# Performance work log

Measured on AMD Instinct MI355X. Metric: run time of the kernel, lower is better.

## Reference

```python
import jax, jax.numpy as jnp
from jax import lax
import numpy as np

NUM_LABELS = 48
BATCH, SEQ_LEN = 512, 1024


def setup_inputs() -> dict:
    key = jax.random.key(0)
    k1, k2, k3, k4, k5 = jax.random.split(key, 5)
    emissions = jax.random.normal(k1, (BATCH, SEQ_LEN, NUM_LABELS), dtype=jnp.float32)
    labels = jax.random.randint(k2, (BATCH, SEQ_LEN), 0, NUM_LABELS, dtype=jnp.int32)
    mask = jnp.ones((BATCH, SEQ_LEN), dtype=jnp.int32)
    transitions = jax.random.normal(k3, (NUM_LABELS, NUM_LABELS), dtype=jnp.float32)
    start_transitions = jax.random.normal(k4, (NUM_LABELS,), dtype=jnp.float32)
    end_transitions = jax.random.normal(k5, (NUM_LABELS,), dtype=jnp.float32)
    return {
        "emissions": emissions,
        "labels": labels,
        "mask": mask,
        "transitions": transitions,
        "start_transitions": start_transitions,
        "end_transitions": end_transitions,
    }


def _gold_score(emissions, labels, mask, transitions, start_transitions, end_transitions):
    maskf = mask.astype(emissions.dtype)
    # emissions gathered at gold labels: (B, T)
    emit = jnp.take_along_axis(emissions, labels[..., None], axis=2)[..., 0]
    # NOTE: original indexes transitions[labels_t, labels_{t-1}] (cur, prev)
    trans = transitions[labels[:, 1:], labels[:, :-1]]  # (B, T-1)
    lengths = jnp.sum(mask, axis=1) - 1  # index of last real token
    last_labels = jnp.take_along_axis(labels, lengths[:, None], axis=1)[:, 0]
    score = (start_transitions[labels[:, 0]] + emit[:, 0]
             + jnp.sum((emit[:, 1:] + trans) * maskf[:, 1:], axis=1)
             + end_transitions[last_labels])
    return score  # (B,)


def _forward_algorithm(emissions, mask, transitions, start_transitions, end_transitions):
    # carry: alpha scores (B, L)
    score0 = start_transitions[None, :] + emissions[:, 0]

    def step(score, xs):
        emit_t, mask_t = xs  # (B, L), (B,)
        # logsumexp over previous label i of score[b,i] + transitions[i,j]
        next_score = jax.nn.logsumexp(score[:, :, None] + transitions[None, :, :], axis=1) + emit_t
        score = jnp.where(mask_t[:, None].astype(bool), next_score, score)
        return score, None

    xs = (jnp.moveaxis(emissions[:, 1:], 1, 0), jnp.moveaxis(mask[:, 1:], 1, 0))
    score, _ = lax.scan(step, score0, xs)
    return jax.nn.logsumexp(score + end_transitions[None, :], axis=1)  # (B,)


def reference(emissions, labels, mask, transitions, start_transitions, end_transitions):
    gold = _gold_score(emissions, labels, mask, transitions, start_transitions, end_transitions)
    fwd = _forward_algorithm(emissions, mask, transitions, start_transitions, end_transitions)
    return jnp.mean(fwd - gold)
```

## Files before the change

### kernel.cpp

```cpp
#include <hip/hip_runtime.h>

constexpr int NL    = 48;
constexpr int SEQ   = 1024;
constexpr int BATCH = 512;

template<int N>
__device__ __forceinline__ float rrf(float x) {
    if constexpr (N == 0) return x;
    else return __int_as_float(
        __builtin_amdgcn_mov_dpp(__float_as_int(x), 0x120 | N, 0xF, 0xF, false));
}
template<int N>
__device__ __forceinline__ unsigned rru(unsigned x) {
    if constexpr (N == 0) return x;
    else return (unsigned)
        __builtin_amdgcn_mov_dpp((int)x, 0x120 | N, 0xF, 0xF, false);
}

#define FMAC_DPP(ACC_, SRC_, COEF_, N_)                                       \
    asm("v_fmac_f32_dpp %0, %1, %2 row_ror:" #N_                              \
        " row_mask:0xf bank_mask:0xf"                                         \
        : "+v"(ACC_) : "v"(SRC_), "v"(COEF_))

__device__ __forceinline__ void spread4(unsigned x,
        unsigned &c, unsigned &d, unsigned &e, unsigned &f) {
    auto rA = __builtin_amdgcn_permlane32_swap(x, x, false, false);
    auto rc = __builtin_amdgcn_permlane16_swap(rA[0], rA[0], false, false);
    auto re = __builtin_amdgcn_permlane16_swap(rA[1], rA[1], false, false);
    c = rc[0]; d = rc[1]; e = re[0]; f = re[1];
}

#define RF3A(N_, x0_, x1_, x2_)                                               \
    FMAC_DPP(x0_, c_, EA[N_], N_);                                            \
    FMAC_DPP(x1_, d_, EB[N_], N_);                                            \
    FMAC_DPP(x2_, e_, EC[N_], N_);
#define RFF(N_, xx_) xx_ = fmaf(rrf<N_>(f_), ED[N_], xx_);

#define CRF_STEP(T_, SLOT_, RN_) do {                                         \
    float ee_ = __expf(embuf[SLOT_]);                                         \
    int   mt_ = (int)((mb_cur >> (SLOT_)) & 1);                               \
    int   tn_ = (T_) + 8; if (tn_ > SEQ - 1) tn_ = SEQ - 1;                   \
    embuf[SLOT_] = em[tn_ * NL + jc];                                         \
    unsigned cu_, du_, eu_, fu_;                                              \
    spread4(__float_as_uint(v), cu_, du_, eu_, fu_);                          \
     \
    asm("s_nop 1" : "+v"(cu_), "+v"(du_), "+v"(eu_));                         \
    float c_ = __uint_as_float(cu_), d_ = __uint_as_float(du_);               \
    float e_ = __uint_as_float(eu_), f_ = __uint_as_float(fu_);               \
    float rm_ = 1.0f;                                                         \
    if (RN_) {                                                                \
        float g_ = fmaxf(fmaxf(c_, d_), fmaxf(e_, f_));                       \
        g_ = fmaxf(g_, rrf<8>(g_));  g_ = fmaxf(g_, rrf<4>(g_));              \
        g_ = fmaxf(g_, rrf<2>(g_));  g_ = fmaxf(g_, rrf<1>(g_));              \
        rm_ = __builtin_amdgcn_rcpf(g_);                                      \
        S += __logf(g_);                                                      \
    }                                                                         \
    float a0_ = c_ * EA[0], a1_ = d_ * EB[0], a2_ = e_ * EC[0];               \
    float a3_ = 0.f, a4_ = 0.f, a5_ = 0.f;                                    \
    RF3A(1,  a3_, a4_, a5_)  RF3A(2,  a0_, a1_, a2_)                          \
    RF3A(3,  a3_, a4_, a5_)  RF3A(4,  a0_, a1_, a2_)                          \
    RF3A(5,  a3_, a4_, a5_)  RF3A(6,  a0_, a1_, a2_)                          \
    RF3A(7,  a3_, a4_, a5_)  RF3A(8,  a0_, a1_, a2_)                          \
    RF3A(9,  a3_, a4_, a5_)  RF3A(10, a0_, a1_, a2_)                          \
    RF3A(11, a3_, a4_, a5_)  RF3A(12, a0_, a1_, a2_)                          \
    RF3A(13, a3_, a4_, a5_)  RF3A(14, a0_, a1_, a2_)                          \
    RF3A(15, a3_, a4_, a5_)                                                   \
    if (useF) {    \
        RFF(0,  a0_) RFF(1,  a1_) RFF(2,  a2_) RFF(3,  a3_)                   \
        RFF(4,  a4_) RFF(5,  a5_) RFF(6,  a0_) RFF(7,  a1_)                   \
        RFF(8,  a2_) RFF(9,  a3_) RFF(10, a4_) RFF(11, a5_)                   \
        RFF(12, a0_) RFF(13, a1_) RFF(14, a2_) RFF(15, a3_)                   \
    }                                                                         \
    float acc_ = ((a0_ + a3_) + (a1_ + a4_)) + (a2_ + a5_);                   \
    v = (mt_ ? acc_ * ee_ : v) * rm_;                                         \
} while (0)

#define EPREP(N_) do {                                                        \
    unsigned i0 = rru<N_>(ic_), i1 = rru<N_>(id_);                            \
    unsigned i2 = rru<N_>(ie_), i3 = rru<N_>(if_);                            \
    EA[N_] = (i0 < (unsigned)NL) ? __expf(trans[i0 * NL + jc]) : 0.0f;        \
    EB[N_] = (i1 < (unsigned)NL) ? __expf(trans[i1 * NL + jc]) : 0.0f;        \
    EC[N_] = (i2 < (unsigned)NL) ? __expf(trans[i2 * NL + jc]) : 0.0f;        \
    ED[N_] = (i3 < (unsigned)NL) ? __expf(trans[i3 * NL + jc]) : 0.0f;        \
} while (0)

__global__ __launch_bounds__(128)
__attribute__((amdgpu_waves_per_eu(1, 1)))
void crf_fused(
    const float* __restrict__ emissions, const int* __restrict__ labels,
    const int* __restrict__ mask, const float* __restrict__ trans,
    const float* __restrict__ startt, const float* __restrict__ endt,
    float* __restrict__ gold_out, float* __restrict__ fwd_out)
{
    const int b   = blockIdx.x;
    const int tid = threadIdx.x;
    const float* em = emissions + (size_t)b * SEQ * NL;
    const int*   mk = mask + b * SEQ;

    if (tid < 64) {
        const int  j   = tid;
        const bool act = (j < NL);
        const int  jc  = act ? j : NL - 1;

        unsigned ic_, id_, ie_, if_;
        spread4((unsigned)j, ic_, id_, ie_, if_);
        const bool useF = (__ballot(if_ < (unsigned)NL) != 0ull);

        float EA[16], EB[16], EC[16], ED[16];
        EPREP(0);  EPREP(1);  EPREP(2);  EPREP(3);
        EPREP(4);  EPREP(5);  EPREP(6);  EPREP(7);
        EPREP(8);  EPREP(9);  EPREP(10); EPREP(11);
        EPREP(12); EPREP(13); EPREP(14); EPREP(15);

        int mval = mk[tid & 7];
        unsigned long long mb_cur = __ballot(mval != 0);
        mval = mk[8 + (tid & 7)];

        float s0 = act ? (startt[jc] + em[jc]) : -3.0e38f;
        float m0 = s0;
        #pragma unroll
        for (int o = 32; o; o >>= 1) m0 = fmaxf(m0, __shfl_xor(m0, o));
        float v = act ? __expf(s0 - m0) : 0.0f;
        float S = m0;

        float embuf[8];
        #pragma unroll
        for (int t = 1; t <= 8; ++t) embuf[t & 7] = em[t * NL + jc];

        CRF_STEP(1, 1, 0); CRF_STEP(2, 2, 0); CRF_STEP(3, 3, 0); CRF_STEP(4, 4, 0);
        CRF_STEP(5, 5, 1); CRF_STEP(6, 6, 0); CRF_STEP(7, 7, 0);

        for (int tb = 8; tb <= SEQ - 8; tb += 8) {
            mb_cur = __ballot(mval != 0);
            int tm = tb + 8 + (tid & 7);
            if (tm > SEQ - 1) tm = SEQ - 1;
            mval = mk[tm];
            CRF_STEP(tb + 0, 0, 1);
            CRF_STEP(tb + 1, 1, 0); CRF_STEP(tb + 2, 2, 0); CRF_STEP(tb + 3, 3, 0);
            CRF_STEP(tb + 4, 4, 1);
            CRF_STEP(tb + 5, 5, 0); CRF_STEP(tb + 6, 6, 0); CRF_STEP(tb + 7, 7, 0);
        }

        float w = act ? v * __expf(endt[jc]) : 0.0f;
        #pragma unroll
        for (int o = 32; o; o >>= 1) w += __shfl_xor(w, o);
        if (j == 0) fwd_out[b] = S + __logf(w);
    } else {
        const int l = tid - 64;
        const int* lb = labels + b * SEQ;

        float part = 0.0f; int mcnt = 0;
        for (int t = l; t < SEQ; t += 64) {
            int lt = lb[t];
            int mt = mk[t];
            mcnt += mt;
            if (t == 0) {
                part += startt[lt] + em[lt];
            } else {
                float e  = em[t * NL + lt];
                float tr = trans[lt * NL + lb[t - 1]];
                if (mt) part += e + tr;
            }
        }
        #pragma unroll
        for (int o = 32; o; o >>= 1) {
            part += __shfl_xor(part, o);
            mcnt += __shfl_xor(mcnt, o);
        }
        if (l == 0) {
            int len = mcnt - 1;
            gold_out[b] = part + endt[lb[len]];
        }
    }
}

__global__ __launch_bounds__(64) void crf_reduce(
    const float* __restrict__ gold, const float* __restrict__ fwd,
    float* __restrict__ out)
{
    const int l = threadIdx.x;
    float s = 0.0f;
    for (int bIdx = l; bIdx < BATCH; bIdx += 64) s += fwd[bIdx] - gold[bIdx];
    #pragma unroll
    for (int o = 32; o; o >>= 1) s += __shfl_xor(s, o);
    if (l == 0) out[0] = s * (1.0f / (float)BATCH);
}

extern "C" void kernel_launch(void* const* d_in, const int* in_sizes, int n_in,
                              void* d_out, int out_size, void* d_ws, size_t ws_size,
                              hipStream_t stream) {
    const float* emissions = (const float*)d_in[0];
    const int*   labels    = (const int*)d_in[1];
    const int*   mask      = (const int*)d_in[2];
    const float* trans     = (const float*)d_in[3];
    const float* startt    = (const float*)d_in[4];
    const float* endt      = (const float*)d_in[5];
    float*       out       = (float*)d_out;
    float*       wsf       = (float*)d_ws;

    crf_fused<<<BATCH, 128, 0, stream>>>(emissions, labels, mask, trans, startt, endt,
                                         wsf, wsf + BATCH);
    crf_reduce<<<1, 64, 0, stream>>>(wsf, wsf + BATCH, out);
}
```

Baseline: 361.4 us.

## Remap labels to lanes so the fourth spread group uses DPP FMAs

Labels are reassigned to lanes so that inactive padding lanes fall into the fourth permlane spread group. The f-group contributions become v_fmac_dpp instructions with no separate DPP moves, and f is dropped from the renormalisation max. The emission prefetch uses a pointer that advances each block, and the last block is peeled so the per-step index clamp goes away. The label remap adds shared-memory setup and depends on the permlane mapping placing every f-lane on an inactive label.

```diff
diff --git a/kernel.cpp b/kernel.cpp
--- a/kernel.cpp
+++ b/kernel.cpp
@@ -34,22 +34,20 @@
     FMAC_DPP(x0_, c_, EA[N_], N_);                                            \
     FMAC_DPP(x1_, d_, EB[N_], N_);                                            \
     FMAC_DPP(x2_, e_, EC[N_], N_);
-#define RFF(N_, xx_) xx_ = fmaf(rrf<N_>(f_), ED[N_], xx_);
-
-#define CRF_STEP(T_, SLOT_, RN_) do {                                         \
+
+#define CRF_STEP(SLOT_, RN_, PF_) do {                                        \
     float ee_ = __expf(embuf[SLOT_]);                                         \
     int   mt_ = (int)((mb_cur >> (SLOT_)) & 1);                               \
-    int   tn_ = (T_) + 8; if (tn_ > SEQ - 1) tn_ = SEQ - 1;                   \
-    embuf[SLOT_] = em[tn_ * NL + jc];                                         \
+    if (PF_) embuf[SLOT_] = emp[(8 + SLOT_) * NL];                            \
     unsigned cu_, du_, eu_, fu_;                                              \
     spread4(__float_as_uint(v), cu_, du_, eu_, fu_);                          \
-     \
+         \
     asm("s_nop 1" : "+v"(cu_), "+v"(du_), "+v"(eu_));                         \
     float c_ = __uint_as_float(cu_), d_ = __uint_as_float(du_);               \
     float e_ = __uint_as_float(eu_), f_ = __uint_as_float(fu_);               \
     float rm_ = 1.0f;                                                         \
     if (RN_) {                                                                \
-        float g_ = fmaxf(fmaxf(c_, d_), fmaxf(e_, f_));                       \
+        float g_ = fmaxf(fmaxf(c_, d_), e_);                                  \
         g_ = fmaxf(g_, rrf<8>(g_));  g_ = fmaxf(g_, rrf<4>(g_));              \
         g_ = fmaxf(g_, rrf<2>(g_));  g_ = fmaxf(g_, rrf<1>(g_));              \
         rm_ = __builtin_amdgcn_rcpf(g_);                                      \
@@ -65,11 +63,16 @@
     RF3A(11, a3_, a4_, a5_)  RF3A(12, a0_, a1_, a2_)                          \
     RF3A(13, a3_, a4_, a5_)  RF3A(14, a0_, a1_, a2_)                          \
     RF3A(15, a3_, a4_, a5_)                                                   \
-    if (useF) {    \
-        RFF(0,  a0_) RFF(1,  a1_) RFF(2,  a2_) RFF(3,  a3_)                   \
-        RFF(4,  a4_) RFF(5,  a5_) RFF(6,  a0_) RFF(7,  a1_)                   \
-        RFF(8,  a2_) RFF(9,  a3_) RFF(10, a4_) RFF(11, a5_)                   \
-        RFF(12, a0_) RFF(13, a1_) RFF(14, a2_) RFF(15, a3_)                   \
+    if (useF) {            \
+        a3_ = fmaf(f_, ED[0], a3_);                                           \
+        FMAC_DPP(a4_, f_, ED[1],  1);  FMAC_DPP(a5_, f_, ED[2],  2);          \
+        FMAC_DPP(a0_, f_, ED[3],  3);  FMAC_DPP(a1_, f_, ED[4],  4);          \
+        FMAC_DPP(a2_, f_, ED[5],  5);  FMAC_DPP(a3_, f_, ED[6],  6);          \
+        FMAC_DPP(a4_, f_, ED[7],  7);  FMAC_DPP(a5_, f_, ED[8],  8);          \
+        FMAC_DPP(a0_, f_, ED[9],  9);  FMAC_DPP(a1_, f_, ED[10], 10);         \
+        FMAC_DPP(a2_, f_, ED[11], 11); FMAC_DPP(a3_, f_, ED[12], 12);         \
+        FMAC_DPP(a4_, f_, ED[13], 13); FMAC_DPP(a5_, f_, ED[14], 14);         \
+        FMAC_DPP(a0_, f_, ED[15], 15);                                        \
     }                                                                         \
     float acc_ = ((a0_ + a3_) + (a1_ + a4_)) + (a2_ + a5_);                   \
     v = (mt_ ? acc_ * ee_ : v) * rm_;                                         \
@@ -97,13 +100,32 @@
     const float* em = emissions + (size_t)b * SEQ * NL;
     const int*   mk = mask + b * SEQ;
 
+    __shared__ int gflag[64];
+
     if (tid < 64) {
-        const int  j   = tid;
-        const bool act = (j < NL);
-        const int  jc  = act ? j : NL - 1;
+        const int j = tid;
+
+        unsigned p0_, p1_, p2_, pf_;
+        spread4((unsigned)j, p0_, p1_, p2_, pf_);
+        gflag[j] = 0;
+        gflag[pf_ & 63] = 1;
+        const int inG = gflag[j];
+        const unsigned long long gball = __ballot(inG != 0);
+        const int gcount = __popcll(gball);
+        const unsigned long long below = (j == 0) ? 0ull : ((~0ull) >> (64 - j));
+
+        unsigned sig;
+        if (gcount <= 16)
+            sig = inG ? 48u + (unsigned)__popcll(gball & below)
+                      : (unsigned)__popcll(~gball & below);
+        else
+            sig = (unsigned)j;
+
+        const bool act = (sig < (unsigned)NL);
+        const int  jc  = act ? (int)sig : NL - 1;
 
         unsigned ic_, id_, ie_, if_;
-        spread4((unsigned)j, ic_, id_, ie_, if_);
+        spread4(sig, ic_, id_, ie_, if_);
         const bool useF = (__ballot(if_ < (unsigned)NL) != 0ull);
 
         float EA[16], EB[16], EC[16], ED[16];
@@ -123,23 +145,30 @@
         float v = act ? __expf(s0 - m0) : 0.0f;
         float S = m0;
 
+        const float* emp = em + jc;
         float embuf[8];
         #pragma unroll
-        for (int t = 1; t <= 8; ++t) embuf[t & 7] = em[t * NL + jc];
-
-        CRF_STEP(1, 1, 0); CRF_STEP(2, 2, 0); CRF_STEP(3, 3, 0); CRF_STEP(4, 4, 0);
-        CRF_STEP(5, 5, 1); CRF_STEP(6, 6, 0); CRF_STEP(7, 7, 0);
-
-        for (int tb = 8; tb <= SEQ - 8; tb += 8) {
+        for (int t = 1; t <= 8; ++t) embuf[t & 7] = emp[t * NL];
+
+        CRF_STEP(1, 0, 1); CRF_STEP(2, 0, 1); CRF_STEP(3, 0, 1); CRF_STEP(4, 0, 1);
+        CRF_STEP(5, 1, 1); CRF_STEP(6, 0, 1); CRF_STEP(7, 0, 1);
+        emp += 8 * NL;
+
+        for (int tb = 8; tb <= SEQ - 16; tb += 8) {
             mb_cur = __ballot(mval != 0);
-            int tm = tb + 8 + (tid & 7);
-            if (tm > SEQ - 1) tm = SEQ - 1;
-            mval = mk[tm];
-            CRF_STEP(tb + 0, 0, 1);
-            CRF_STEP(tb + 1, 1, 0); CRF_STEP(tb + 2, 2, 0); CRF_STEP(tb + 3, 3, 0);
-            CRF_STEP(tb + 4, 4, 1);
-            CRF_STEP(tb + 5, 5, 0); CRF_STEP(tb + 6, 6, 0); CRF_STEP(tb + 7, 7, 0);
-        }
+            mval = mk[tb + 8 + (tid & 7)];
+            CRF_STEP(0, 1, 1);
+            CRF_STEP(1, 0, 1); CRF_STEP(2, 0, 1); CRF_STEP(3, 0, 1);
+            CRF_STEP(4, 1, 1);
+            CRF_STEP(5, 0, 1); CRF_STEP(6, 0, 1); CRF_STEP(7, 0, 1);
+            emp += 8 * NL;
+        }
+
+        mb_cur = __ballot(mval != 0);
+        CRF_STEP(0, 1, 0);
+        CRF_STEP(1, 0, 0); CRF_STEP(2, 0, 0); CRF_STEP(3, 0, 0);
+        CRF_STEP(4, 1, 0);
+        CRF_STEP(5, 0, 0); CRF_STEP(6, 0, 0); CRF_STEP(7, 0, 0);
 
         float w = act ? v * __expf(endt[jc]) : 0.0f;
         #pragma unroll
```

Measured after the change: 349.1 us. 3.4% less time.
